# Optimization experiments

Measured on AMD Instinct MI355X. Metric: run time of the kernel, lower is better.

## Reference

```python
import jax, jax.numpy as jnp
import numpy as np
import math

B, Q, K, D = 16, 2048, 2048, 128


def setup_inputs() -> dict:
    key = jax.random.key(0)
    k1, k2, k3, k4 = jax.random.split(key, 4)
    return {
        "queries": jax.random.normal(k1, (B, Q, D), dtype=jnp.float32),
        "keys": jax.random.normal(k2, (B, K, D), dtype=jnp.float32),
        "values": jax.random.normal(k3, (B, K, D), dtype=jnp.float32),
        "valid_lens": jax.random.randint(k4, (B,), 1, K + 1, dtype=jnp.int32),
    }


def reference(queries, keys, values, valid_lens):
    d = queries.shape[2]
    # scores: [B, Q, K]
    scores = jnp.einsum("bqd,bkd->bqk", queries, keys) / math.sqrt(d)
    # mask: arange(K) < valid_lens[b], broadcast over query dim -> [B, 1, K]
    mask = jnp.arange(scores.shape[-1])[None, None, :] < valid_lens[:, None, None]
    scores = jnp.where(mask, scores, jnp.float32(-1000000.0))
    weights = jax.nn.softmax(scores, axis=-1)
    return jnp.einsum("bqk,bkd->bqd", weights, values)
```

## Files before the change

### kernel.cpp

```cpp
#include <hip/hip_runtime.h>

typedef unsigned short u16;
typedef __bf16 bf16x8 __attribute__((ext_vector_type(8)));
typedef float f32x4 __attribute__((ext_vector_type(4)));

union B8 { uint4 u; bf16x8 v; };
union U8 { u16 s[8]; uint4 u; };

#define NQ 2048
#define NK 2048
#define ND 128

template<int C>
__device__ __forceinline__ float dppf(float x) {
  int v = __builtin_bit_cast(int, x);
  int r = __builtin_amdgcn_update_dpp(v, v, C, 0xF, 0xF, true);
  return __builtin_bit_cast(float, r);
}
__device__ __forceinline__ float rowmax16(float x) {
  x = fmaxf(x, dppf<0xB1>(x));
  x = fmaxf(x, dppf<0x4E>(x));
  x = fmaxf(x, dppf<0x141>(x));
  x = fmaxf(x, dppf<0x140>(x));
  return x;
}
__device__ __forceinline__ float rowsum16(float x) {
  x += dppf<0xB1>(x);
  x += dppf<0x4E>(x);
  x += dppf<0x141>(x);
  x += dppf<0x140>(x);
  return x;
}

__device__ __forceinline__ bf16x8 cvt8(float4 a, float4 b) {
  bf16x8 r;
  r[0] = (__bf16)a.x; r[1] = (__bf16)a.y; r[2] = (__bf16)a.z; r[3] = (__bf16)a.w;
  r[4] = (__bf16)b.x; r[5] = (__bf16)b.y; r[6] = (__bf16)b.z; r[7] = (__bf16)b.w;
  return r;
}

__device__ __forceinline__ void async16(const u16* g, u16* l) {
  __builtin_amdgcn_global_load_lds(
      (const __attribute__((address_space(1))) unsigned int*)g,
      (__attribute__((address_space(3))) unsigned int*)l, 16, 0, 0);
}

constexpr float CEXP = 0.08838834764831845f * 1.44269504088896340f;

__global__ __launch_bounds__(256)
void prepack(const float* __restrict__ kg, const float* __restrict__ vg,
             u16* __restrict__ wk, u16* __restrict__ wvp)
{
  __shared__ __align__(16) u16 sVp[8192];
  const int bt  = blockIdx.x;
  const int tid = threadIdx.x;
  const int srow = tid >> 2, scq = tid & 3;
  const size_t rowoff = (size_t)((bt >> 5) * NK + (bt & 31) * 64 + srow) * ND + scq * 32;

  u16* kimg = wk + (size_t)bt * 8192;
  {
    const float* src = kg + rowoff;
    #pragma unroll
    for (int c = 0; c < 4; ++c) {
      B8 tt; tt.v = cvt8(*(const float4*)(src + c * 8), *(const float4*)(src + c * 8 + 4));
      *(uint4*)(&kimg[srow * 128 + (((scq * 4 + c) ^ (srow & 15)) << 3)]) = tt.u;
    }
  }
  {
    const float* src = vg + rowoff;
    #pragma unroll
    for (int c = 0; c < 4; ++c) {
      B8 x; x.v = cvt8(*(const float4*)(src + c * 8), *(const float4*)(src + c * 8 + 4));
      U8 tt; tt.u = x.u;
      #pragma unroll
      for (int j = 0; j < 8; ++j) {
        int d = scq * 32 + c * 8 + j;
        sVp[d * 64 + (((srow >> 3) ^ j) << 3) + (srow & 7)] = tt.s[j];
      }
    }
  }
  __syncthreads();
  u16* vimg = wvp + (size_t)bt * 8192;
  const uint4* s4 = (const uint4*)sVp;
  uint4* d4 = (uint4*)vimg;
  #pragma unroll
  for (int k = 0; k < 4; ++k) d4[tid + 256 * k] = s4[tid + 256 * k];
}

__global__ __launch_bounds__(512, 4)
void flash_chunk(const float* __restrict__ qg, const int* __restrict__ vlg,
                 const u16* __restrict__ wk, const u16* __restrict__ wvp,
                 float* __restrict__ pO, float* __restrict__ pML)
{
  __shared__ __align__(16) u16 sK[2][8192];
  __shared__ __align__(16) u16 sV[2][8192];
  __shared__ __align__(16) u16 sP[8][1024];

  const int tid  = threadIdx.x;
  const int lane = tid & 63;
  const int wv   = tid >> 6;
  const int n    = lane & 15;
  const int quad = lane >> 4;

  const int bi   = blockIdx.x;
  const int b    = ((bi & 7) << 1) | ((bi >> 3) & 1);
  const int rest = bi >> 4;
  const int qt   = rest & 15;
  const int ck   = rest >> 4;

  const int vl = vlg[b];
  const int nt = (vl + 63) >> 6;
  const int t0 = ck * 8;
  if (t0 >= nt) return;
  const int t1 = (t0 + 8 < nt) ? (t0 + 8) : nt;

  const int qrow0 = qt * 128 + wv * 16;

  bf16x8 qf[4];
  #pragma unroll
  for (int c = 0; c < 4; ++c) {
    const float* qp = qg + (size_t)(b * NQ + qrow0 + n) * ND + c * 32 + quad * 8;
    qf[c] = cvt8(*(const float4*)qp, *(const float4*)(qp + 4));
  }

  f32x4 O[8];
  float mst[4], lst[4];
  #pragma unroll
  for (int f = 0; f < 8; ++f) O[f] = (f32x4){0.f, 0.f, 0.f, 0.f};
  #pragma unroll
  for (int r = 0; r < 4; ++r) { mst[r] = -__builtin_inff(); lst[r] = 0.f; }

  #define STAGE(t, buf)                                                        \
    do {                                                                       \
      const size_t io_ = (size_t)(b * 32 + (t)) * 8192 + wv * 1024;            \
      const u16* gk_ = wk  + io_ + lane * 8;                                   \
      const u16* gv_ = wvp + io_ + lane * 8;                                   \
      u16* lk_ = sK[(buf)] + wv * 1024 + lane * 8;                             \
      u16* lv_ = sV[(buf)] + wv * 1024 + lane * 8;                             \
      async16(gk_,       lk_);                                                 \
      async16(gk_ + 512, lk_ + 512);                                           \
      async16(gv_,       lv_);                                                 \
      async16(gv_ + 512, lv_ + 512);                                           \
    } while (0)

  u16* const Pw = sP[wv];

  STAGE(t0, 0);

  for (int t = t0; t < t1; ++t) {
    __syncthreads();
    if (t + 1 < t1) STAGE(t + 1, (t - t0 + 1) & 1);

    const u16* Kg = sK[(t - t0) & 1];
    const u16* Vg = sV[(t - t0) & 1];

    f32x4 S[4];
    #pragma unroll
    for (int jn = 0; jn < 4; ++jn) S[jn] = (f32x4){0.f, 0.f, 0.f, 0.f};
    #pragma unroll
    for (int c = 0; c < 4; ++c)
      #pragma unroll
      for (int jn = 0; jn < 4; ++jn) {
        B8 bb;
        bb.u = *(const uint4*)(&Kg[(jn * 16 + n) * 128 + (((c * 4 + quad) ^ n) << 3)]);
        S[jn] = __builtin_amdgcn_mfma_f32_16x16x32_bf16(qf[c], bb.v, S[jn], 0, 0, 0);
      }

    if (t * 64 + 64 > vl) {
      #pragma unroll
      for (int jn = 0; jn < 4; ++jn) {
        const bool msk = (t * 64 + jn * 16 + n) >= vl;
        #pragma unroll
        for (int r = 0; r < 4; ++r)
          S[jn][r] = msk ? -1e30f : S[jn][r];
      }
    }

    float al[4];
    #pragma unroll
    for (int r = 0; r < 4; ++r) {
      float mx = fmaxf(fmaxf(S[0][r], S[1][r]), fmaxf(S[2][r], S[3][r]));
      mx = rowmax16(mx);
      float mnew = fmaxf(mst[r], mx);
      float a = __builtin_exp2f((mst[r] - mnew) * CEXP);
      mst[r] = mnew;
      float ssum = 0.f;
      #pragma unroll
      for (int jn = 0; jn < 4; ++jn) {
        float p = __builtin_exp2f((S[jn][r] - mnew) * CEXP);
        S[jn][r] = p;
        ssum += p;
      }
      ssum = rowsum16(ssum);
      lst[r] = lst[r] * a + ssum;
      al[r] = a;
    }
    #pragma unroll
    for (int f = 0; f < 8; ++f) {
      O[f][0] *= al[0]; O[f][1] *= al[1]; O[f][2] *= al[2]; O[f][3] *= al[3];
    }

    #pragma unroll
    for (int jn = 0; jn < 4; ++jn)
      #pragma unroll
      for (int r = 0; r < 4; ++r) {
        int row = quad * 4 + r;
        __bf16 h = (__bf16)S[jn][r];
        Pw[row * 64 + (((jn * 2 + (n >> 3)) ^ (row & 7)) << 3) + (n & 7)]
            = __builtin_bit_cast(u16, h);
      }

    #pragma unroll
    for (int kc = 0; kc < 2; ++kc) {
      B8 ta;
      ta.u = *(const uint4*)(&Pw[n * 64 + (((kc * 4 + quad) ^ (n & 7)) << 3)]);
      bf16x8 af = ta.v;
      #pragma unroll
      for (int f = 0; f < 8; ++f) {
        int d = f * 16 + n;
        B8 bb;
        bb.u = *(const uint4*)(&Vg[d * 64 + (((kc * 4 + quad) ^ (n & 7)) << 3)]);
        O[f] = __builtin_amdgcn_mfma_f32_16x16x32_bf16(af, bb.v, O[f], 0, 0, 0);
      }
    }
  }
  #undef STAGE

  const size_t ti = (size_t)((b * 16 + qt) * 4 + ck);
  float* po = pO + ti * 16384;
  #pragma unroll
  for (int f = 0; f < 8; ++f)
    #pragma unroll
    for (int r = 0; r < 4; ++r)
      po[(wv * 16 + quad * 4 + r) * 128 + f * 16 + n] = O[f][r];
  if (n == 0) {
    float* ps = pML + ti * 256;
    #pragma unroll
    for (int r = 0; r < 4; ++r) {
      const int row = wv * 16 + quad * 4 + r;
      ps[row * 2]     = mst[r];
      ps[row * 2 + 1] = lst[r];
    }
  }
}

__global__ __launch_bounds__(256)
void merge_chunks(const int* __restrict__ vlg, const float* __restrict__ pO,
                  const float* __restrict__ pML, float* __restrict__ og)
{
  __shared__ float w[128][4];
  const int tid = threadIdx.x;
  const int bi  = blockIdx.x;
  const int b   = ((bi & 7) << 1) | ((bi >> 3) & 1);
  const int qt  = bi >> 4;

  const int vl = vlg[b];
  const int nt = (vl + 63) >> 6;
  const int nc = (nt + 7) >> 3;
  const size_t ti0 = (size_t)(b * 16 + qt) * 4;

  if (tid < 128) {
    const int row = tid;
    float m[4], l[4];
    float mx = -__builtin_inff();
    for (int c = 0; c < nc; ++c) {
      m[c] = pML[(ti0 + c) * 256 + row * 2];
      l[c] = pML[(ti0 + c) * 256 + row * 2 + 1];
      mx = fmaxf(mx, m[c]);
    }
    float L = 0.f;
    float a[4];
    for (int c = 0; c < nc; ++c) {
      a[c] = __builtin_exp2f((m[c] - mx) * CEXP);
      L += l[c] * a[c];
    }
    const float inv = 1.0f / L;
    #pragma unroll
    for (int c = 0; c < 4; ++c)
      w[row][c] = (c < nc) ? a[c] * inv : 0.f;
  }
  __syncthreads();

  const float4* p4 = (const float4*)(pO + ti0 * 16384);
  float4* o4 = (float4*)(og + (size_t)(b * NQ + qt * 128) * ND);
  #pragma unroll
  for (int it = 0; it < 16; ++it) {
    const int gi  = it * 256 + tid;
    const int row = gi >> 5;
    float4 acc = {0.f, 0.f, 0.f, 0.f};
    for (int c = 0; c < nc; ++c) {
      const float4 x = p4[c * 4096 + gi];
      const float s = w[row][c];
      acc.x += x.x * s; acc.y += x.y * s; acc.z += x.z * s; acc.w += x.w * s;
    }
    o4[gi] = acc;
  }
}

__global__ __launch_bounds__(512, 2)
void flash_fwd(const float* __restrict__ qg, const int* __restrict__ vlg,
               float* __restrict__ og,
               const u16* __restrict__ wk, const u16* __restrict__ wvp)
{
  __shared__ __align__(16) u16 smem[81920];
  u16* const sKb = smem;
  u16* const sVb = smem + 32768;
  u16* const sPb = smem + 65536;
  float* const fb = (float*)smem;

  const int tid  = threadIdx.x;
  const int lane = tid & 63;
  const int wv   = tid >> 6;
  const int qw   = wv & 3;
  const int grp  = wv >> 2;
  const int n    = lane & 15;
  const int quad = lane >> 4;

  const int bi = blockIdx.x;
  const int b  = ((bi & 7) << 1) | ((bi >> 3) & 1);
  const int qt = bi >> 4;

  const int vl = vlg[b];
  const int nt = (vl + 63) >> 6;
  const int qrow0 = qt * 128 + qw * 32;

  bf16x8 qf[2][4];
  #pragma unroll
  for (int mb = 0; mb < 2; ++mb)
    #pragma unroll
    for (int c = 0; c < 4; ++c) {
      const float* qp = qg + (size_t)(b * NQ + qrow0 + mb * 16 + n) * ND + c * 32 + quad * 8;
      qf[mb][c] = cvt8(*(const float4*)qp, *(const float4*)(qp + 4));
    }

  f32x4 O[2][8];
  float mst[2][4], lst[2][4];
  #pragma unroll
  for (int mb = 0; mb < 2; ++mb) {
    #pragma unroll
    for (int f = 0; f < 8; ++f) O[mb][f] = (f32x4){0.f, 0.f, 0.f, 0.f};
    #pragma unroll
    for (int r = 0; r < 4; ++r) { mst[mb][r] = -__builtin_inff(); lst[mb][r] = 0.f; }
  }

  #define STAGE(t, buf)                                                        \
    do {                                                                       \
      const size_t io_ = (size_t)(b * 32 + (t)) * 8192 + qw * 2048;            \
      const u16* gk_ = wk  + io_ + lane * 8;                                   \
      const u16* gv_ = wvp + io_ + lane * 8;                                   \
      u16* lk_ = sKb + (grp * 2 + (buf)) * 8192 + qw * 2048;                   \
      u16* lv_ = sVb + (grp * 2 + (buf)) * 8192 + qw * 2048;                   \
      _Pragma("unroll")                                                        \
      for (int j_ = 0; j_ < 4; ++j_) {                                         \
        async16(gk_ + j_ * 512, lk_ + j_ * 512 + lane * 8);                    \
        async16(gv_ + j_ * 512, lv_ + j_ * 512 + lane * 8);                    \
      }                                                                        \
    } while (0)

  u16* const Pw = sPb + wv * 2048;

  if (grp < nt) STAGE(grp, 0);

  const int NS = (nt + 1) >> 1;
  for (int i = 0; i < NS; ++i) {
    __syncthreads();
    const int t  = 2 * i + grp;
    const int tn = t + 2;
    if (tn < nt) STAGE(tn, (i + 1) & 1);

    if (t < nt) {
      const u16* Kg = sKb + (grp * 2 + (i & 1)) * 8192;
      const u16* Vg = sVb + (grp * 2 + (i & 1)) * 8192;

      f32x4 S[2][4];
      #pragma unroll
      for (int mb = 0; mb < 2; ++mb)
        #pragma unroll
        for (int jn = 0; jn < 4; ++jn) S[mb][jn] = (f32x4){0.f, 0.f, 0.f, 0.f};
      #pragma unroll
      for (int c = 0; c < 4; ++c)
        #pragma unroll
        for (int jn = 0; jn < 4; ++jn) {
          B8 bb;
          bb.u = *(const uint4*)(&Kg[(jn * 16 + n) * 128 + (((c * 4 + quad) ^ n) << 3)]);
          S[0][jn] = __builtin_amdgcn_mfma_f32_16x16x32_bf16(qf[0][c], bb.v, S[0][jn], 0, 0, 0);
          S[1][jn] = __builtin_amdgcn_mfma_f32_16x16x32_bf16(qf[1][c], bb.v, S[1][jn], 0, 0, 0);
        }

      if (t * 64 + 64 > vl) {
        #pragma unroll
        for (int jn = 0; jn < 4; ++jn) {
          const bool msk = (t * 64 + jn * 16 + n) >= vl;
          #pragma unroll
          for (int r = 0; r < 4; ++r) {
            S[0][jn][r] = msk ? -1e30f : S[0][jn][r];
            S[1][jn][r] = msk ? -1e30f : S[1][jn][r];
          }
        }
      }

      float al[2][4];
      #pragma unroll
      for (int mb = 0; mb < 2; ++mb)
        #pragma unroll
        for (int r = 0; r < 4; ++r) {
          float mx = fmaxf(fmaxf(S[mb][0][r], S[mb][1][r]), fmaxf(S[mb][2][r], S[mb][3][r]));
          mx = rowmax16(mx);
          float mnew = fmaxf(mst[mb][r], mx);
          float a = __builtin_exp2f((mst[mb][r] - mnew) * CEXP);
          mst[mb][r] = mnew;
          float ssum = 0.f;
          #pragma unroll
          for (int jn = 0; jn < 4; ++jn) {
            float p = __builtin_exp2f((S[mb][jn][r] - mnew) * CEXP);
            S[mb][jn][r] = p;
            ssum += p;
          }
          ssum = rowsum16(ssum);
          lst[mb][r] = lst[mb][r] * a + ssum;
          al[mb][r] = a;
        }
      #pragma unroll
      for (int mb = 0; mb < 2; ++mb)
        #pragma unroll
        for (int f = 0; f < 8; ++f) {
          O[mb][f][0] *= al[mb][0]; O[mb][f][1] *= al[mb][1];
          O[mb][f][2] *= al[mb][2]; O[mb][f][3] *= al[mb][3];
        }

      #pragma unroll
      for (int mb = 0; mb < 2; ++mb)
        #pragma unroll
        for (int jn = 0; jn < 4; ++jn)
          #pragma unroll
          for (int r = 0; r < 4; ++r) {
            int row = mb * 16 + quad * 4 + r;
            __bf16 h = (__bf16)S[mb][jn][r];
            Pw[row * 64 + (((jn * 2 + (n >> 3)) ^ (row & 7)) << 3) + (n & 7)]
                = __builtin_bit_cast(u16, h);
          }

      #pragma unroll
      for (int kc = 0; kc < 2; ++kc) {
        bf16x8 af[2];
        #pragma unroll
        for (int mb = 0; mb < 2; ++mb) {
          B8 ta;
          ta.u = *(const uint4*)(&Pw[(mb * 16 + n) * 64 + (((kc * 4 + quad) ^ (n & 7)) << 3)]);
          af[mb] = ta.v;
        }
        #pragma unroll
        for (int f = 0; f < 8; ++f) {
          int d = f * 16 + n;
          B8 bb;
          bb.u = *(const uint4*)(&Vg[d * 64 + (((kc * 4 + quad) ^ (n & 7)) << 3)]);
          O[0][f] = __builtin_amdgcn_mfma_f32_16x16x32_bf16(af[0], bb.v, O[0][f], 0, 0, 0);
          O[1][f] = __builtin_amdgcn_mfma_f32_16x16x32_bf16(af[1], bb.v, O[1][f], 0, 0, 0);
        }
      }
    }
  }
  #undef STAGE

  __syncthreads();
  float* const ps = fb + 16384;
  if (grp == 1) {
    #pragma unroll
    for (int mb = 0; mb < 2; ++mb) {
      #pragma unroll
      for (int f = 0; f < 8; ++f)
        #pragma unroll
        for (int r = 0; r < 4; ++r)
          fb[(qw * 32 + mb * 16 + quad * 4 + r) * 128 + f * 16 + n] = O[mb][f][r];
      if (n == 0) {
        #pragma unroll
        for (int r = 0; r < 4; ++r) {
          const int row = qw * 32 + mb * 16 + quad * 4 + r;
          ps[row * 2]     = mst[mb][r];
          ps[row * 2 + 1] = lst[mb][r];
        }
      }
    }
  }
  __syncthreads();
  if (grp == 0) {
    #pragma unroll
    for (int mb = 0; mb < 2; ++mb)
      #pragma unroll
      for (int r = 0; r < 4; ++r) {
        const int row = qw * 32 + mb * 16 + quad * 4 + r;
        const float m1 = ps[row * 2], l1 = ps[row * 2 + 1];
        const float m  = fmaxf(mst[mb][r], m1);
        const float a0 = __builtin_exp2f((mst[mb][r] - m) * CEXP);
        const float a1 = __builtin_exp2f((m1 - m) * CEXP);
        const float rl = 1.0f / (lst[mb][r] * a0 + l1 * a1);
        #pragma unroll
        for (int f = 0; f < 8; ++f) {
          const int idx = row * 128 + f * 16 + n;
          fb[idx] = (O[mb][f][r] * a0 + fb[idx] * a1) * rl;
        }
      }
  }
  __syncthreads();
  {
    const float4* s4 = (const float4*)fb;
    float4* d4 = (float4*)(og + (size_t)(b * NQ + qt * 128) * ND);
    #pragma unroll
    for (int k = 0; k < 8; ++k)
      d4[tid + 512 * k] = s4[tid + 512 * k];
  }
}

__global__ __launch_bounds__(1024)
void flash_fwd_fb(const float* __restrict__ qg, const float* __restrict__ kg,
                  const float* __restrict__ vg, const int* __restrict__ vlg,
                  float* __restrict__ og)
{
  __shared__ __align__(16) u16 sK[2][64 * 128];
  __shared__ __align__(16) u16 sV[2][64 * 128];
  __shared__ __align__(16) u16 sP[16][16 * 64];

  const int tid  = threadIdx.x;
  const int lane = tid & 63;
  const int wv   = tid >> 6;
  const int qw   = wv & 7;
  const int grp  = wv >> 3;
  const int n    = lane & 15;
  const int quad = lane >> 4;

  const int bi = blockIdx.x;
  const int b  = ((bi & 7) << 1) | ((bi >> 3) & 1);
  const int qt = bi >> 4;

  const int vl = vlg[b];
  const int nt = (vl + 63) >> 6;
  const int qrow0 = qt * 128 + qw * 16;

  bf16x8 qf[4];
  #pragma unroll
  for (int c = 0; c < 4; ++c) {
    const float* qp = qg + (size_t)(b * NQ + qrow0 + n) * ND + c * 32 + quad * 8;
    qf[c] = cvt8(*(const float4*)qp, *(const float4*)(qp + 4));
  }

  f32x4 O[8];
  float mst[4], lst[4];
  #pragma unroll
  for (int f = 0; f < 8; ++f) O[f] = (f32x4){0.f, 0.f, 0.f, 0.f};
  #pragma unroll
  for (int r = 0; r < 4; ++r) { mst[r] = -__builtin_inff(); lst[r] = 0.f; }

  const float* kb = kg + (size_t)(b * NK) * ND;
  const float* vb = vg + (size_t)(b * NK) * ND;
  const int stid = tid & 511;
  const int srow = stid >> 3, sc8 = stid & 7;
  bf16x8 kreg[2], vreg[2];

  auto kload = [&](int t) {
    const float* src = kb + (size_t)(t * 64 + srow) * ND + sc8 * 16;
    #pragma unroll
    for (int c = 0; c < 2; ++c)
      kreg[c] = cvt8(*(const float4*)(src + c * 8), *(const float4*)(src + c * 8 + 4));
  };
  auto kstore = [&]() {
    #pragma unroll
    for (int c = 0; c < 2; ++c) {
      B8 tt; tt.v = kreg[c];
      *(uint4*)(&sK[grp][srow * 128 + (((sc8 * 2 + c) ^ (srow & 15)) << 3)]) = tt.u;
    }
  };
  auto vload = [&](int t) {
    const float* src = vb + (size_t)(t * 64 + srow) * ND + sc8 * 16;
    #pragma unroll
    for (int c = 0; c < 2; ++c)
      vreg[c] = cvt8(*(const float4*)(src + c * 8), *(const float4*)(src + c * 8 + 4));
  };
  auto vstore = [&]() {
    #pragma unroll
    for (int c = 0; c < 2; ++c) {
      B8 x; x.v = vreg[c];
      U8 tt; tt.u = x.u;
      #pragma unroll
      for (int j = 0; j < 8; ++j) {
        int d = sc8 * 16 + c * 8 + j;
        sV[grp][d * 64 + (((srow >> 3) ^ j) << 3) + (srow & 7)] = tt.s[j];
      }
    }
  };

  if (grp < nt) { kload(grp); vload(grp); kstore(); vstore(); }

  u16* Pw = sP[wv];
  const u16* Kg = sK[grp];
  const u16* Vg = sV[grp];

  const int NS = (nt + 1) >> 1;
  for (int i = 0; i < NS; ++i) {
    __syncthreads();
    const int t  = 2 * i + grp;
    const int tn = t + 2;
    if (tn < nt) { kload(tn); vload(tn); }

    if (t < nt) {
      f32x4 S[4];
      #pragma unroll
      for (int jn = 0; jn < 4; ++jn) S[jn] = (f32x4){0.f, 0.f, 0.f, 0.f};
      #pragma unroll
      for (int c = 0; c < 4; ++c)
        #pragma unroll
        for (int jn = 0; jn < 4; ++jn) {
          B8 bb;
          bb.u = *(const uint4*)(&Kg[(jn * 16 + n) * 128 + (((c * 4 + quad) ^ n) << 3)]);
          S[jn] = __builtin_amdgcn_mfma_f32_16x16x32_bf16(qf[c], bb.v, S[jn], 0, 0, 0);
        }
      if (t * 64 + 64 > vl) {
        #pragma unroll
        for (int jn = 0; jn < 4; ++jn) {
          const bool msk = (t * 64 + jn * 16 + n) >= vl;
          #pragma unroll
          for (int r = 0; r < 4; ++r)
            S[jn][r] = msk ? -1e30f : S[jn][r];
        }
      }
      float al[4];
      #pragma unroll
      for (int r = 0; r < 4; ++r) {
        float mx = fmaxf(fmaxf(S[0][r], S[1][r]), fmaxf(S[2][r], S[3][r]));
        mx = rowmax16(mx);
        float mnew = fmaxf(mst[r], mx);
        float a = __builtin_exp2f((mst[r] - mnew) * CEXP);
        mst[r] = mnew;
        float ssum = 0.f;
        #pragma unroll
        for (int jn = 0; jn < 4; ++jn) {
          float p = __builtin_exp2f((S[jn][r] - mnew) * CEXP);
          S[jn][r] = p;
          ssum += p;
        }
        ssum = rowsum16(ssum);
        lst[r] = lst[r] * a + ssum;
        al[r] = a;
      }
      #pragma unroll
      for (int f = 0; f < 8; ++f) {
        O[f][0] *= al[0]; O[f][1] *= al[1]; O[f][2] *= al[2]; O[f][3] *= al[3];
      }
      #pragma unroll
      for (int jn = 0; jn < 4; ++jn)
        #pragma unroll
        for (int r = 0; r < 4; ++r) {
          int row = quad * 4 + r;
          __bf16 h = (__bf16)S[jn][r];
          Pw[row * 64 + (((jn * 2 + (n >> 3)) ^ (row & 7)) << 3) + (n & 7)]
              = __builtin_bit_cast(u16, h);
        }
      #pragma unroll
      for (int kc = 0; kc < 2; ++kc) {
        B8 ta;
        ta.u = *(const uint4*)(&Pw[n * 64 + (((kc * 4 + quad) ^ (n & 7)) << 3)]);
        bf16x8 af = ta.v;
        #pragma unroll
        for (int f = 0; f < 8; ++f) {
          int d = f * 16 + n;
          B8 bb;
          bb.u = *(const uint4*)(&Vg[d * 64 + (((kc * 4 + quad) ^ (n & 7)) << 3)]);
          O[f] = __builtin_amdgcn_mfma_f32_16x16x32_bf16(af, bb.v, O[f], 0, 0, 0);
        }
      }
    }
    __syncthreads();
    if (tn < nt) { kstore(); vstore(); }
  }

  if (grp == 1) {
    float* ob = ((qw < 4) ? (float*)sK : (float*)sV) + (qw & 3) * 2048 + lane * 32;
    #pragma unroll
    for (int f = 0; f < 8; ++f)
      #pragma unroll
      for (int r = 0; r < 4; ++r)
        ob[f * 4 + r] = O[f][r];
    float* sb = (float*)sP + qw * 512 + lane * 8;
    #pragma unroll
    for (int r = 0; r < 4; ++r) { sb[r] = mst[r]; sb[4 + r] = lst[r]; }
  }
  __syncthreads();
  if (grp == 0) {
    const float* ob = ((qw < 4) ? (const float*)sK : (const float*)sV) + (qw & 3) * 2048 + lane * 32;
    const float* sb = (const float*)sP + qw * 512 + lane * 8;
    #pragma unroll
    for (int r = 0; r < 4; ++r) {
      const float m1 = sb[r], l1 = sb[4 + r];
      const float m  = fmaxf(mst[r], m1);
      const float a0 = __builtin_exp2f((mst[r] - m) * CEXP);
      const float a1 = __builtin_exp2f((m1 - m) * CEXP);
      const float rl = 1.0f / (lst[r] * a0 + l1 * a1);
      const int qrow = qrow0 + quad * 4 + r;
      float* op = og + (size_t)(b * NQ + qrow) * ND + n;
      #pragma unroll
      for (int f = 0; f < 8; ++f)
        op[f * 16] = (O[f][r] * a0 + ob[f * 4 + r] * a1) * rl;
    }
  }
}

extern "C" void kernel_launch(void* const* d_in, const int* in_sizes, int n_in,
                              void* d_out, int out_size, void* d_ws, size_t ws_size,
                              hipStream_t stream) {
  const float* q  = (const float*)d_in[0];
  const float* k  = (const float*)d_in[1];
  const float* v  = (const float*)d_in[2];
  const int*  vl  = (const int*)d_in[3];
  float* out = (float*)d_out;

  const size_t need_img   = (size_t)16 * 1024 * 1024;
  const size_t need_split = need_img + (size_t)(64 + 1) * 1024 * 1024;

  if (ws_size >= need_split) {
    u16*   wk  = (u16*)d_ws;
    u16*   wvv = wk + 4194304;
    float* pO  = (float*)((char*)d_ws + need_img);
    float* pML = (float*)((char*)d_ws + need_img + (size_t)64 * 1024 * 1024);
    hipLaunchKernelGGL(prepack, dim3(512), dim3(256), 0, stream, k, v, wk, wvv);
    hipLaunchKernelGGL(flash_chunk, dim3(1024), dim3(512), 0, stream,
                       q, vl, wk, wvv, pO, pML);
    hipLaunchKernelGGL(merge_chunks, dim3(256), dim3(256), 0, stream,
                       vl, pO, pML, out);
  } else if (ws_size >= need_img) {
    u16* wk  = (u16*)d_ws;
    u16* wvv = wk + 4194304;
    hipLaunchKernelGGL(prepack, dim3(512), dim3(256), 0, stream, k, v, wk, wvv);
    hipLaunchKernelGGL(flash_fwd, dim3(256), dim3(512), 0, stream, q, vl, out, wk, wvv);
  } else {
    hipLaunchKernelGGL(flash_fwd_fb, dim3(256), dim3(1024), 0, stream, q, k, v, vl, out);
  }
}
```

Baseline: 172.8 us.

## Fuse chunk merge into flash kernel via atomic last-block and 32-row waves

After: 308.1 us. +78.3%, slower.

```diff
diff --git a/kernel.cpp b/kernel.cpp
--- a/kernel.cpp
+++ b/kernel.cpp
@@ -87,14 +87,15 @@
   for (int k = 0; k < 4; ++k) d4[tid + 256 * k] = s4[tid + 256 * k];
 }
 
-__global__ __launch_bounds__(512, 4)
-void flash_chunk(const float* __restrict__ qg, const int* __restrict__ vlg,
-                 const u16* __restrict__ wk, const u16* __restrict__ wvp,
-                 float* __restrict__ pO, float* __restrict__ pML)
+__global__ __launch_bounds__(256, 2)
+void flash_chunk2(const float* __restrict__ qg, const int* __restrict__ vlg,
+                  const u16* __restrict__ wk, const u16* __restrict__ wvp,
+                  float* __restrict__ pO, float* __restrict__ pML,
+                  int* __restrict__ done, float* __restrict__ og)
 {
   __shared__ __align__(16) u16 sK[2][8192];
   __shared__ __align__(16) u16 sV[2][8192];
-  __shared__ __align__(16) u16 sP[8][1024];
+  __shared__ __align__(16) u16 sP[4][2048];
 
   const int tid  = threadIdx.x;
   const int lane = tid & 63;
@@ -104,43 +105,49 @@
 
   const int bi   = blockIdx.x;
   const int b    = ((bi & 7) << 1) | ((bi >> 3) & 1);
-  const int rest = bi >> 4;
-  const int qt   = rest & 15;
-  const int ck   = rest >> 4;
+  const int qt   = (bi >> 4) & 15;
+  const int ck   = bi >> 8;
 
   const int vl = vlg[b];
   const int nt = (vl + 63) >> 6;
   const int t0 = ck * 8;
   if (t0 >= nt) return;
   const int t1 = (t0 + 8 < nt) ? (t0 + 8) : nt;
-
-  const int qrow0 = qt * 128 + wv * 16;
-
-  bf16x8 qf[4];
-  #pragma unroll
-  for (int c = 0; c < 4; ++c) {
-    const float* qp = qg + (size_t)(b * NQ + qrow0 + n) * ND + c * 32 + quad * 8;
-    qf[c] = cvt8(*(const float4*)qp, *(const float4*)(qp + 4));
-  }
-
-  f32x4 O[8];
-  float mst[4], lst[4];
-  #pragma unroll
-  for (int f = 0; f < 8; ++f) O[f] = (f32x4){0.f, 0.f, 0.f, 0.f};
-  #pragma unroll
-  for (int r = 0; r < 4; ++r) { mst[r] = -__builtin_inff(); lst[r] = 0.f; }
+  const int nc = (nt + 7) >> 3;
+
+  const int qrow0 = qt * 128 + wv * 32;
+
+  bf16x8 qf[2][4];
+  #pragma unroll
+  for (int mb = 0; mb < 2; ++mb)
+    #pragma unroll
+    for (int c = 0; c < 4; ++c) {
+      const float* qp = qg + (size_t)(b * NQ + qrow0 + mb * 16 + n) * ND + c * 32 + quad * 8;
+      qf[mb][c] = cvt8(*(const float4*)qp, *(const float4*)(qp + 4));
+    }
+
+  f32x4 O[2][8];
+  float mst[2][4], lst[2][4];
+  #pragma unroll
+  for (int mb = 0; mb < 2; ++mb) {
+    #pragma unroll
+    for (int f = 0; f < 8; ++f) O[mb][f] = (f32x4){0.f, 0.f, 0.f, 0.f};
+    #pragma unroll
+    for (int r = 0; r < 4; ++r) { mst[mb][r] = -__builtin_inff(); lst[mb][r] = 0.f; }
+  }
 
   #define STAGE(t, buf)                                                        \
     do {                                                                       \
-      const size_t io_ = (size_t)(b * 32 + (t)) * 8192 + wv * 1024;            \
+      const size_t io_ = (size_t)(b * 32 + (t)) * 8192 + wv * 2048;            \
       const u16* gk_ = wk  + io_ + lane * 8;                                   \
       const u16* gv_ = wvp + io_ + lane * 8;                                   \
-      u16* lk_ = sK[(buf)] + wv * 1024 + lane * 8;                             \
-      u16* lv_ = sV[(buf)] + wv * 1024 + lane * 8;                             \
-      async16(gk_,       lk_);                                                 \
-      async16(gk_ + 512, lk_ + 512);                                           \
-      async16(gv_,       lv_);                                                 \
-      async16(gv_ + 512, lv_ + 512);                                           \
+      u16* lk_ = sK[(buf)] + wv * 2048 + lane * 8;                             \
+      u16* lv_ = sV[(buf)] + wv * 2048 + lane * 8;                             \
+      _Pragma("unroll")                                                        \
+      for (int j_ = 0; j_ < 4; ++j_) {                                         \
+        async16(gk_ + j_ * 512, lk_ + j_ * 512);                               \
+        async16(gv_ + j_ * 512, lv_ + j_ * 512);                               \
+      }                                                                        \
     } while (0)
 
   u16* const Pw = sP[wv];
@@ -154,16 +161,19 @@
     const u16* Kg = sK[(t - t0) & 1];
     const u16* Vg = sV[(t - t0) & 1];
 
-    f32x4 S[4];
-    #pragma unroll
-    for (int jn = 0; jn < 4; ++jn) S[jn] = (f32x4){0.f, 0.f, 0.f, 0.f};
+    f32x4 S[2][4];
+    #pragma unroll
+    for (int mb = 0; mb < 2; ++mb)
+      #pragma unroll
+      for (int jn = 0; jn < 4; ++jn) S[mb][jn] = (f32x4){0.f, 0.f, 0.f, 0.f};
     #pragma unroll
     for (int c = 0; c < 4; ++c)
       #pragma unroll
       for (int jn = 0; jn < 4; ++jn) {
         B8 bb;
         bb.u = *(const uint4*)(&Kg[(jn * 16 + n) * 128 + (((c * 4 + quad) ^ n) << 3)]);
-        S[jn] = __builtin_amdgcn_mfma_f32_16x16x32_bf16(qf[c], bb.v, S[jn], 0, 0, 0);
+        S[0][jn] = __builtin_amdgcn_mfma_f32_16x16x32_bf16(qf[0][c], bb.v, S[0][jn], 0, 0, 0);
+        S[1][jn] = __builtin_amdgcn_mfma_f32_16x16x32_bf16(qf[1][c], bb.v, S[1][jn], 0, 0, 0);
       }
 
     if (t * 64 + 64 > vl) {
@@ -171,94 +181,125 @@
       for (int jn = 0; jn < 4; ++jn) {
         const bool msk = (t * 64 + jn * 16 + n) >= vl;
         #pragma unroll
-        for (int r = 0; r < 4; ++r)
-          S[jn][r] = msk ? -1e30f : S[jn][r];
-      }
-    }
-
-    float al[4];
-    #pragma unroll
-    for (int r = 0; r < 4; ++r) {
-      float mx = fmaxf(fmaxf(S[0][r], S[1][r]), fmaxf(S[2][r], S[3][r]));
-      mx = rowmax16(mx);
-      float mnew = fmaxf(mst[r], mx);
-      float a = __builtin_exp2f((mst[r] - mnew) * CEXP);
-      mst[r] = mnew;
-      float ssum = 0.f;
-      #pragma unroll
-      for (int jn = 0; jn < 4; ++jn) {
-        float p = __builtin_exp2f((S[jn][r] - mnew) * CEXP);
-        S[jn][r] = p;
-        ssum += p;
-      }
-      ssum = rowsum16(ssum);
-      lst[r] = lst[r] * a + ssum;
-      al[r] = a;
-    }
-    #pragma unroll
-    for (int f = 0; f < 8; ++f) {
-      O[f][0] *= al[0]; O[f][1] *= al[1]; O[f][2] *= al[2]; O[f][3] *= al[3];
-    }
-
-    #pragma unroll
-    for (int jn = 0; jn < 4; ++jn)
+        for (int r = 0; r < 4; ++r) {
+          S[0][jn][r] = msk ? -1e30f : S[0][jn][r];
+          S[1][jn][r] = msk ? -1e30f : S[1][jn][r];
+        }
+      }
+    }
+
+    float al[2][4];
+    #pragma unroll
+    for (int mb = 0; mb < 2; ++mb)
       #pragma unroll
       for (int r = 0; r < 4; ++r) {
-        int row = quad * 4 + r;
-        __bf16 h = (__bf16)S[jn][r];
-        Pw[row * 64 + (((jn * 2 + (n >> 3)) ^ (row & 7)) << 3) + (n & 7)]
-            = __builtin_bit_cast(u16, h);
-      }
+        float mx = fmaxf(fmaxf(S[mb][0][r], S[mb][1][r]), fmaxf(S[mb][2][r], S[mb][3][r]));
+        mx = rowmax16(mx);
+        float mnew = fmaxf(mst[mb][r], mx);
+        float a = __builtin_exp2f((mst[mb][r] - mnew) * CEXP);
+        mst[mb][r] = mnew;
+        float ssum = 0.f;
+        #pragma unroll
+        for (int jn = 0; jn < 4; ++jn) {
+          float p = __builtin_exp2f((S[mb][jn][r] - mnew) * CEXP);
+          S[mb][jn][r] = p;
+          ssum += p;
+        }
+        ssum = rowsum16(ssum);
+        lst[mb][r] = lst[mb][r] * a + ssum;
+        al[mb][r] = a;
+      }
+    #pragma unroll
+    for (int mb = 0; mb < 2; ++mb)
+      #pragma unroll
+      for (int f = 0; f < 8; ++f) {
+        O[mb][f][0] *= al[mb][0]; O[mb][f][1] *= al[mb][1];
+        O[mb][f][2] *= al[mb][2]; O[mb][f][3] *= al[mb][3];
+      }
+
+    #pragma unroll
+    for (int mb = 0; mb < 2; ++mb)
+      #pragma unroll
+      for (int jn = 0; jn < 4; ++jn)
+        #pragma unroll
+        for (int r = 0; r < 4; ++r) {
+          int row = mb * 16 + quad * 4 + r;
+          __bf16 h = (__bf16)S[mb][jn][r];
+          Pw[row * 64 + (((jn * 2 + (n >> 3)) ^ (row & 7)) << 3) + (n & 7)]
+              = __builtin_bit_cast(u16, h);
+        }
 
     #pragma unroll
     for (int kc = 0; kc < 2; ++kc) {
-      B8 ta;
-      ta.u = *(const uint4*)(&Pw[n * 64 + (((kc * 4 + quad) ^ (n & 7)) << 3)]);
-      bf16x8 af = ta.v;
+      bf16x8 af[2];
+      #pragma unroll
+      for (int mb = 0; mb < 2; ++mb) {
+        B8 ta;
+        ta.u = *(const uint4*)(&Pw[(mb * 16 + n) * 64 + (((kc * 4 + quad) ^ (n & 7)) << 3)]);
+        af[mb] = ta.v;
+      }
       #pragma unroll
       for (int f = 0; f < 8; ++f) {
         int d = f * 16 + n;
         B8 bb;
         bb.u = *(const uint4*)(&Vg[d * 64 + (((kc * 4 + quad) ^ (n & 7)) << 3)]);
-        O[f] = __builtin_amdgcn_mfma_f32_16x16x32_bf16(af, bb.v, O[f], 0, 0, 0);
+        O[0][f] = __builtin_amdgcn_mfma_f32_16x16x32_bf16(af[0], bb.v, O[0][f], 0, 0, 0);
+        O[1][f] = __builtin_amdgcn_mfma_f32_16x16x32_bf16(af[1], bb.v, O[1][f], 0, 0, 0);
       }
     }
   }
   #undef STAGE
+
+  if (nc == 1) {
+    #pragma unroll
+    for (int mb = 0; mb < 2; ++mb)
+      #pragma unroll
+      for (int r = 0; r < 4; ++r) {
+        const float rl = 1.0f / lst[mb][r];
+        const int qrow = qrow0 + mb * 16 + quad * 4 + r;
+        float* op = og + (size_t)(b * NQ + qrow) * ND + n;
+        #pragma unroll
+        for (int f = 0; f < 8; ++f)
+          op[f * 16] = O[mb][f][r] * rl;
+      }
+    return;
+  }
 
   const size_t ti = (size_t)((b * 16 + qt) * 4 + ck);
   float* po = pO + ti * 16384;
   #pragma unroll
-  for (int f = 0; f < 8; ++f)
-    #pragma unroll
-    for (int r = 0; r < 4; ++r)
-      po[(wv * 16 + quad * 4 + r) * 128 + f * 16 + n] = O[f][r];
+  for (int mb = 0; mb < 2; ++mb)
+    #pragma unroll
+    for (int f = 0; f < 8; ++f)
+      #pragma unroll
+      for (int r = 0; r < 4; ++r)
+        po[(wv * 32 + mb * 16 + quad * 4 + r) * 128 + f * 16 + n] = O[mb][f][r];
   if (n == 0) {
     float* ps = pML + ti * 256;
     #pragma unroll
-    for (int r = 0; r < 4; ++r) {
-      const int row = wv * 16 + quad * 4 + r;
-      ps[row * 2]     = mst[r];
-      ps[row * 2 + 1] = lst[r];
-    }
-  }
-}
-
-__global__ __launch_bounds__(256)
-void merge_chunks(const int* __restrict__ vlg, const float* __restrict__ pO,
-                  const float* __restrict__ pML, float* __restrict__ og)
-{
-  __shared__ float w[128][4];
-  const int tid = threadIdx.x;
-  const int bi  = blockIdx.x;
-  const int b   = ((bi & 7) << 1) | ((bi >> 3) & 1);
-  const int qt  = bi >> 4;
-
-  const int vl = vlg[b];
-  const int nt = (vl + 63) >> 6;
-  const int nc = (nt + 7) >> 3;
+    for (int mb = 0; mb < 2; ++mb)
+      #pragma unroll
+      for (int r = 0; r < 4; ++r) {
+        const int row = wv * 32 + mb * 16 + quad * 4 + r;
+        ps[row * 2]     = mst[mb][r];
+        ps[row * 2 + 1] = lst[mb][r];
+      }
+  }
+
+  float* const wts   = (float*)sP;
+  int*   const winfl = (int*)sP + 512;
+
+  __threadfence();
+  __syncthreads();
+  if (tid == 0) {
+    const int old = atomicAdd(&done[b * 16 + qt], 1);
+    *winfl = (old + 1 == nc);
+  }
+  __syncthreads();
+  if (!*winfl) return;
+  __threadfence();
+
   const size_t ti0 = (size_t)(b * 16 + qt) * 4;
-
   if (tid < 128) {
     const int row = tid;
     float m[4], l[4];
@@ -277,7 +318,7 @@
     const float inv = 1.0f / L;
     #pragma unroll
     for (int c = 0; c < 4; ++c)
-      w[row][c] = (c < nc) ? a[c] * inv : 0.f;
+      wts[row * 4 + c] = (c < nc) ? a[c] * inv : 0.f;
   }
   __syncthreads();
 
@@ -290,7 +331,7 @@
     float4 acc = {0.f, 0.f, 0.f, 0.f};
     for (int c = 0; c < nc; ++c) {
       const float4 x = p4[c * 4096 + gi];
-      const float s = w[row][c];
+      const float s = wts[row * 4 + c];
       acc.x += x.x * s; acc.y += x.y * s; acc.z += x.z * s; acc.w += x.w * s;
     }
     o4[gi] = acc;
@@ -713,18 +754,18 @@
   float* out = (float*)d_out;
 
   const size_t need_img   = (size_t)16 * 1024 * 1024;
-  const size_t need_split = need_img + (size_t)(64 + 1) * 1024 * 1024;
+  const size_t need_split = (size_t)82 * 1024 * 1024;
 
   if (ws_size >= need_split) {
     u16*   wk  = (u16*)d_ws;
     u16*   wvv = wk + 4194304;
     float* pO  = (float*)((char*)d_ws + need_img);
-    float* pML = (float*)((char*)d_ws + need_img + (size_t)64 * 1024 * 1024);
+    float* pML = (float*)((char*)d_ws + (size_t)80 * 1024 * 1024);
+    int*   dn  = (int*)  ((char*)d_ws + (size_t)81 * 1024 * 1024);
+    hipMemsetAsync(dn, 0, 1024, stream);
     hipLaunchKernelGGL(prepack, dim3(512), dim3(256), 0, stream, k, v, wk, wvv);
-    hipLaunchKernelGGL(flash_chunk, dim3(1024), dim3(512), 0, stream,
-                       q, vl, wk, wvv, pO, pML);
-    hipLaunchKernelGGL(merge_chunks, dim3(256), dim3(256), 0, stream,
-                       vl, pO, pML, out);
+    hipLaunchKernelGGL(flash_chunk2, dim3(1024), dim3(256), 0, stream,
+                       q, vl, wk, wvv, pO, pML, dn, out);
   } else if (ws_size >= need_img) {
     u16* wk  = (u16*)d_ws;
     u16* wvv = wk + 4194304;
```
